# Performance work log

Hardware: AMD Instinct MI355X
Metric: run time of the kernel (lower is better)

The kernel has to match this reference:

```python
import jax, jax.numpy as jnp
import numpy as np

NUM_MODES = 256
IN_FEATURES = 256
OUT_FEATURES = 64
LAYERS = 256   # brick-wall mesh depth
PAIRS = 128    # disjoint adjacent-mode pairs per layer
BATCH = 131072


def setup_inputs() -> dict:
    key = jax.random.key(0)
    kx, kt, kp, ko = jax.random.split(key, 4)
    x = jax.random.normal(kx, (BATCH, IN_FEATURES), dtype=jnp.float32)
    theta = jax.random.uniform(kt, (LAYERS, PAIRS), dtype=jnp.float32, minval=0.0, maxval=float(np.pi))
    phi = jax.random.uniform(kp, (LAYERS, PAIRS), dtype=jnp.float32, minval=0.0, maxval=float(2 * np.pi))
    output_phases = jax.random.uniform(ko, (NUM_MODES,), dtype=jnp.float32, minval=0.0, maxval=float(2 * np.pi))
    # Clements-style brick-wall layout: even layers pair (0,1),(2,3),...;
    # odd layers pair (1,2),(3,4),... with a periodic wrap pair (255,0).
    m1 = np.zeros((LAYERS, PAIRS), np.int32)
    m2 = np.zeros((LAYERS, PAIRS), np.int32)
    for l in range(LAYERS):
        idx = (l % 2 + 2 * np.arange(PAIRS)) % NUM_MODES
        m1[l] = idx
        m2[l] = (idx + 1) % NUM_MODES
    return {
        "x": x,
        "theta": theta,
        "phi": phi,
        "output_phases": output_phases,
        "mode1": jnp.asarray(m1),
        "mode2": jnp.asarray(m2),
    }


def _normalize_optical_params(theta, phi):
    # theta -> [0, pi/2], phi -> [0, 2pi), mirroring normalize_optical_params
    theta = theta % np.pi
    flip = theta > (np.pi / 2)
    theta = jnp.where(flip, np.pi - theta, theta)
    phi = jnp.where(flip, phi + np.pi, phi) % (2.0 * np.pi)
    return theta, phi


def _build_transformation(theta, phi, output_phases, mode1, mode2):
    """Compose the interferometer unitary U = D(out_phases) * T_K * ... * T_1,
    where each T_k is a beamsplitter Givens rotation:
      T[m1,m1]=e^{i phi} cos(t), T[m1,m2]=-sin(t),
      T[m2,m1]=e^{i phi} sin(t), T[m2,m2]= cos(t).
    Pairs within one layer are disjoint, so a whole layer is applied at once."""
    theta, phi = _normalize_optical_params(theta, phi)
    U0 = jnp.eye(NUM_MODES, dtype=jnp.complex64)

    def layer(U, inputs):
        m1, m2, th, ph = inputs              # each [PAIRS]
        r1, r2 = U[m1], U[m2]                # [PAIRS, NUM_MODES]
        e = jnp.exp(1j * ph)[:, None]        # complex64 [PAIRS, 1]
        c = jnp.cos(th)[:, None]
        s = jnp.sin(th)[:, None]
        U = U.at[m1].set(e * c * r1 - s * r2)
        U = U.at[m2].set(e * s * r1 + c * r2)
        return U, None

    U, _ = jax.lax.scan(layer, U0, (mode1, mode2, theta, phi))
    U = jnp.exp(1j * output_phases)[:, None] * U
    return jnp.real(U).astype(jnp.float32)   # [NUM_MODES, NUM_MODES]


def reference(x, theta, phi, output_phases, mode1, mode2):
    T = _build_transformation(theta, phi, output_phases, mode1, mode2)
    # input mask is all-ones (in_features == num_modes); output mask keeps the
    # first OUT_FEATURES modes, then output is sliced to OUT_FEATURES, which
    # is equivalent to using the first OUT_FEATURES rows of T directly.
    T_eff = T[:OUT_FEATURES]                 # [OUT_FEATURES, NUM_MODES]
    return x @ T_eff.T                       # [BATCH, OUT_FEATURES]
```

## Files before the change

kernel.cpp:

```cpp
#include <hip/hip_runtime.h>
#include <hip/hip_bf16.h>
#include <cstdint>
#include <cstddef>

#define PI_F 3.14159265358979323846f
#define TWO_PI_F 6.28318530717958647692f

typedef __bf16 bf16x8 __attribute__((ext_vector_type(8)));
typedef __bf16 bf16x4 __attribute__((ext_vector_type(4)));
typedef float  f32x4  __attribute__((ext_vector_type(4)));

__device__ __forceinline__ __bf16 to_bf16(float f) { return (__bf16)f; }

#define GLD_LDS16(gsrc, ldst)                                            \
  __builtin_amdgcn_global_load_lds(                                      \
      (const __attribute__((address_space(1))) void*)(gsrc),             \
      (__attribute__((address_space(3))) void*)(ldst), 16, 0, 0)

__global__ __launch_bounds__(256) void olk_params(
    const float* __restrict__ theta, const float* __restrict__ phi,
    float4* __restrict__ t4, float2* __restrict__ t2) {
  int idx = blockIdx.x * 256 + threadIdx.x;
  float t = fmodf(theta[idx], PI_F);
  float p = phi[idx];
  if (t > 0.5f * PI_F) { t = PI_F - t; p += PI_F; }
  p = fmodf(p, TWO_PI_F);
  float c  = cosf(t), s  = sinf(t);
  float cp = cosf(p), sp = sinf(p);
  t4[idx] = make_float4(cp * c, sp * c, cp * s, sp * s);
  t2[idx] = make_float2(c, s);
}

struct P8 {
  float4 qa[8];
  float4 qb[8];
  float4 cc[8];
};

template<bool TBL>
__device__ __forceinline__ void loadP8(P8& P, int lb, int lane,
    const float4* __restrict__ t4, const float2* __restrict__ t2,
    const float* __restrict__ theta, const float* __restrict__ phi) {
  if (TBL) {
#pragma unroll
    for (int k = 0; k < 8; ++k) {
      int idx = (lb + k) * 128 + 2 * lane;
      P.qa[k] = t4[idx];
      P.qb[k] = t4[idx + 1];
      P.cc[k] = *(const float4*)&t2[idx];
    }
  } else {
#pragma unroll
    for (int k = 0; k < 8; ++k) {
      int idx = (lb + k) * 128 + 2 * lane;
      float2 th = *(const float2*)&theta[idx];
      float2 ph = *(const float2*)&phi[idx];
      float ta = fmodf(th.x, PI_F), pa = ph.x;
      if (ta > 0.5f * PI_F) { ta = PI_F - ta; pa += PI_F; }
      pa = fmodf(pa, TWO_PI_F);
      float tb = fmodf(th.y, PI_F), pb = ph.y;
      if (tb > 0.5f * PI_F) { tb = PI_F - tb; pb += PI_F; }
      pb = fmodf(pb, TWO_PI_F);
      float ca = cosf(ta), sa = sinf(ta), cpa = cosf(pa), spa = sinf(pa);
      float cb = cosf(tb), sb = sinf(tb), cpb = cosf(pb), spb = sinf(pb);
      P.qa[k] = make_float4(cpa * ca, spa * ca, cpa * sa, spa * sa);
      P.qb[k] = make_float4(cpb * cb, spb * cb, cpb * sb, spb * sb);
      P.cc[k] = make_float4(ca, sa, cb, sb);
    }
  }
}

__device__ __forceinline__ void layer_step(bool odd, int lane,
    float4 qa, float4 qb, float4 cc,
    float& vre0, float& vim0, float& vre1, float& vim1,
    float& vre2, float& vim2, float& vre3, float& vim3) {
  if (!odd) {
    float nr0 = qa.x * vre0 - qa.y * vim0 + qa.z * vre1 - qa.w * vim1;
    float ni0 = qa.x * vim0 + qa.y * vre0 + qa.z * vim1 + qa.w * vre1;
    float nr1 = cc.x * vre1 - cc.y * vre0;
    float ni1 = cc.x * vim1 - cc.y * vim0;
    float nr2 = qb.x * vre2 - qb.y * vim2 + qb.z * vre3 - qb.w * vim3;
    float ni2 = qb.x * vim2 + qb.y * vre2 + qb.z * vim3 + qb.w * vre3;
    float nr3 = cc.z * vre3 - cc.w * vre2;
    float ni3 = cc.z * vim3 - cc.w * vim2;
    vre0 = nr0; vim0 = ni0; vre1 = nr1; vim1 = ni1;
    vre2 = nr2; vim2 = ni2; vre3 = nr3; vim3 = ni3;
  } else {
    int nxt = (lane + 1) & 63, prv = (lane + 63) & 63;
    float xre = __shfl(vre0, nxt, 64);
    float xim = __shfl(vim0, nxt, 64);
    float pre = __shfl(vre3, prv, 64);
    float pim = __shfl(vim3, prv, 64);
    float cp  = __shfl(cc.z, prv, 64);
    float sp  = __shfl(cc.w, prv, 64);
    float nr1 = qa.x * vre1 - qa.y * vim1 + qa.z * vre2 - qa.w * vim2;
    float ni1 = qa.x * vim1 + qa.y * vre1 + qa.z * vim2 + qa.w * vre2;
    float nr2 = cc.x * vre2 - cc.y * vre1;
    float ni2 = cc.x * vim2 - cc.y * vim1;
    float nr3 = qb.x * vre3 - qb.y * vim3 + qb.z * xre - qb.w * xim;
    float ni3 = qb.x * vim3 + qb.y * vre3 + qb.z * xim + qb.w * xre;
    float nr0 = cp * vre0 - sp * pre;
    float ni0 = cp * vim0 - sp * pim;
    vre0 = nr0; vim0 = ni0; vre1 = nr1; vim1 = ni1;
    vre2 = nr2; vim2 = ni2; vre3 = nr3; vim3 = ni3;
  }
}

template<bool TBL>
__global__ __launch_bounds__(256) void olk_build(
    const float* __restrict__ theta, const float* __restrict__ phi,
    const float* __restrict__ outph,
    const float4* __restrict__ t4, const float2* __restrict__ t2,
    __bf16* __restrict__ Tb2) {
  int lane = threadIdx.x & 63;
  int r = blockIdx.x * 4 + (threadIdx.x >> 6);
  int c0 = lane * 4;
  float vre0 = (c0 + 0 == r) ? 1.f : 0.f, vim0 = 0.f;
  float vre1 = (c0 + 1 == r) ? 1.f : 0.f, vim1 = 0.f;
  float vre2 = (c0 + 2 == r) ? 1.f : 0.f, vim2 = 0.f;
  float vre3 = (c0 + 3 == r) ? 1.f : 0.f, vim3 = 0.f;

  P8 A, B;
  loadP8<TBL>(A, 31 * 8, lane, t4, t2, theta, phi);
  for (int it = 0; it < 16; ++it) {
    int bA = 31 - 2 * it;
    int bB = bA - 1;
    loadP8<TBL>(B, bB * 8, lane, t4, t2, theta, phi);
#pragma unroll
    for (int k = 7; k >= 0; --k)
      layer_step((k & 1) != 0, lane, A.qa[k], A.qb[k], A.cc[k],
                 vre0, vim0, vre1, vim1, vre2, vim2, vre3, vim3);
    if (it < 15)
      loadP8<TBL>(A, (bB - 1) * 8, lane, t4, t2, theta, phi);
#pragma unroll
    for (int k = 7; k >= 0; --k)
      layer_step((k & 1) != 0, lane, B.qa[k], B.qb[k], B.cc[k],
                 vre0, vim0, vre1, vim1, vre2, vim2, vre3, vim3);
  }

  float oph = outph[r];
  float co = cosf(oph), so = sinf(oph);
  bf16x4 o;
  o[0] = to_bf16(co * vre0 - so * vim0);
  o[1] = to_bf16(co * vre1 - so * vim1);
  o[2] = to_bf16(co * vre2 - so * vim2);
  o[3] = to_bf16(co * vre3 - so * vim3);

  int ks = lane >> 3, sub = lane & 7;
  int pos = ks * 32 + (sub & 3) * 8 + (sub >> 2) * 4;
  *(bf16x4*)(Tb2 + r * 256 + pos) = o;
}

union FragA { bf16x8 v; };

__global__ __launch_bounds__(256, 4) void olk_mm(
    const float* __restrict__ x, const __bf16* __restrict__ Tb2,
    float* __restrict__ out) {
  __shared__ __bf16 Bl[32 * 512];
  int tid = threadIdx.x, lane = tid & 63, w = tid >> 6;
  int l15 = lane & 15, lg = lane >> 4;

#pragma unroll
  for (int j = 0; j < 8; ++j) {
    int idx = w * 8 + j;
    int ks = idx >> 2, nt = idx & 3;
    const __bf16* src = Tb2 + (nt * 16 + l15) * 256 + ks * 32 + lg * 8;
    GLD_LDS16(src, &Bl[idx * 512]);
  }
  __syncthreads();

#pragma unroll 1
  for (int t = 0; t < 2; ++t) {
    int mt = (blockIdx.x * 4 + w) * 2 + t;
    const float* xr = x + ((size_t)(mt * 16 + l15) << 8) + 4 * lg;

    float4 lo[8], hi[8];
#pragma unroll
    for (int ks = 0; ks < 8; ++ks) {
      lo[ks] = *(const float4*)(xr + ks * 32);
      hi[ks] = *(const float4*)(xr + ks * 32 + 16);
    }

    unsigned bb = 0;
    asm volatile("" : "+v"(bb));

    f32x4 acc[4];
#pragma unroll
    for (int nt = 0; nt < 4; ++nt) acc[nt] = (f32x4){0.f, 0.f, 0.f, 0.f};

#pragma unroll
    for (int ks = 0; ks < 8; ++ks) {
      FragA a;
      a.v[0] = to_bf16(lo[ks].x); a.v[1] = to_bf16(lo[ks].y);
      a.v[2] = to_bf16(lo[ks].z); a.v[3] = to_bf16(lo[ks].w);
      a.v[4] = to_bf16(hi[ks].x); a.v[5] = to_bf16(hi[ks].y);
      a.v[6] = to_bf16(hi[ks].z); a.v[7] = to_bf16(hi[ks].w);
#pragma unroll
      for (int nt = 0; nt < 4; ++nt) {
        bf16x8 bv = *(const bf16x8*)&Bl[bb + (ks * 4 + nt) * 512 + lane * 8];
        acc[nt] = __builtin_amdgcn_mfma_f32_16x16x32_bf16(a.v, bv, acc[nt], 0, 0, 0);
      }
    }

    float* ob = out + ((size_t)mt * 16) * 64 + l15;
#pragma unroll
    for (int r = 0; r < 4; ++r)
#pragma unroll
      for (int nt = 0; nt < 4; ++nt)
        ob[(4 * lg + r) * 64 + nt * 16] = acc[nt][r];
  }
}

extern "C" void kernel_launch(void* const* d_in, const int* in_sizes, int n_in,
                              void* d_out, int out_size, void* d_ws, size_t ws_size,
                              hipStream_t stream) {
  const float* x     = (const float*)d_in[0];
  const float* theta = (const float*)d_in[1];
  const float* phi   = (const float*)d_in[2];
  const float* outph = (const float*)d_in[3];
  float* out = (float*)d_out;

  char* ws = (char*)d_ws;
  bool tbl = ws_size >= (size_t)(832 * 1024);
  float4* t4 = (float4*)ws;
  float2* t2 = (float2*)(ws + 512 * 1024);
  __bf16* Tb2 = (__bf16*)(ws + (tbl ? 768 * 1024 : 0));

  if (tbl) {
    olk_params<<<128, 256, 0, stream>>>(theta, phi, t4, t2);
    olk_build<true><<<16, 256, 0, stream>>>(theta, phi, outph, t4, t2, Tb2);
  } else {
    olk_build<false><<<16, 256, 0, stream>>>(theta, phi, outph, nullptr, nullptr, Tb2);
  }
  olk_mm<<<1024, 256, 0, stream>>>(x, Tb2, out);
}
```

Measured before the change: 83.28 us.

## Restructure GEMM into single-wave persistent blocks with double-buffered LDS x staging

```diff
diff --git a/kernel.cpp b/kernel.cpp
--- a/kernel.cpp
+++ b/kernel.cpp
@@ -151,58 +151,66 @@
   *(bf16x4*)(Tb2 + r * 256 + pos) = o;
 }
 
-union FragA { bf16x8 v; };
-
-__global__ __launch_bounds__(256, 4) void olk_mm(
+#define NTILES 8192
+#define NBLK   1280
+#define TQ     6
+#define TAILB  512
+
+__global__ __launch_bounds__(64) void olk_mm(
     const float* __restrict__ x, const __bf16* __restrict__ Tb2,
     float* __restrict__ out) {
-  __shared__ __bf16 Bl[32 * 512];
-  int tid = threadIdx.x, lane = tid & 63, w = tid >> 6;
-  int l15 = lane & 15, lg = lane >> 4;
-
-#pragma unroll
-  for (int j = 0; j < 8; ++j) {
-    int idx = w * 8 + j;
-    int ks = idx >> 2, nt = idx & 3;
-    const __bf16* src = Tb2 + (nt * 16 + l15) * 256 + ks * 32 + lg * 8;
-    GLD_LDS16(src, &Bl[idx * 512]);
-  }
-  __syncthreads();
-
+  __shared__ float4 sb[2][1024];
+  int lane = threadIdx.x;
+  int l15 = lane & 15, lg = lane >> 4, sw = l15 & 7;
+
+  bf16x8 b[8][4];
+#pragma unroll
+  for (int ks = 0; ks < 8; ++ks)
+#pragma unroll
+    for (int nt = 0; nt < 4; ++nt)
+      b[ks][nt] = *(const bf16x8*)(Tb2 + (nt * 16 + l15) * 256 + ks * 32 + lg * 8);
+  asm volatile("s_waitcnt vmcnt(0)" ::: "memory");
+
+  int bid = blockIdx.x;
+  int start, cnt;
+  if (bid < TAILB) { start = bid * (TQ + 1); cnt = TQ + 1; }
+  else             { start = TAILB * (TQ + 1) + (bid - TAILB) * TQ; cnt = TQ; }
+
+  auto stage = [&](int slot, int tile) {
+    const float* base = x + ((size_t)tile << 12);
+#pragma unroll
+    for (int i = 0; i < 16; ++i) {
+      const float* src = base + i * 256 + ((lane ^ (i & 7)) << 2);
+      GLD_LDS16(src, &sb[slot][i * 64]);
+    }
+  };
+
+  stage(0, start);
 #pragma unroll 1
-  for (int t = 0; t < 2; ++t) {
-    int mt = (blockIdx.x * 4 + w) * 2 + t;
-    const float* xr = x + ((size_t)(mt * 16 + l15) << 8) + 4 * lg;
-
-    float4 lo[8], hi[8];
+  for (int t = 0; t < cnt; ++t) {
+    if (t + 1 < cnt) stage((t + 1) & 1, start + t + 1);
+    asm volatile("s_waitcnt vmcnt(16)" ::: "memory");
+
+    const float4* A = sb[t & 1];
+    f32x4 acc[4];
+#pragma unroll
+    for (int nt = 0; nt < 4; ++nt) acc[nt] = (f32x4){0.f, 0.f, 0.f, 0.f};
+
 #pragma unroll
     for (int ks = 0; ks < 8; ++ks) {
-      lo[ks] = *(const float4*)(xr + ks * 32);
-      hi[ks] = *(const float4*)(xr + ks * 32 + 16);
-    }
-
-    unsigned bb = 0;
-    asm volatile("" : "+v"(bb));
-
-    f32x4 acc[4];
-#pragma unroll
-    for (int nt = 0; nt < 4; ++nt) acc[nt] = (f32x4){0.f, 0.f, 0.f, 0.f};
-
-#pragma unroll
-    for (int ks = 0; ks < 8; ++ks) {
-      FragA a;
-      a.v[0] = to_bf16(lo[ks].x); a.v[1] = to_bf16(lo[ks].y);
-      a.v[2] = to_bf16(lo[ks].z); a.v[3] = to_bf16(lo[ks].w);
-      a.v[4] = to_bf16(hi[ks].x); a.v[5] = to_bf16(hi[ks].y);
-      a.v[6] = to_bf16(hi[ks].z); a.v[7] = to_bf16(hi[ks].w);
-#pragma unroll
-      for (int nt = 0; nt < 4; ++nt) {
-        bf16x8 bv = *(const bf16x8*)&Bl[bb + (ks * 4 + nt) * 512 + lane * 8];
-        acc[nt] = __builtin_amdgcn_mfma_f32_16x16x32_bf16(a.v, bv, acc[nt], 0, 0, 0);
-      }
-    }
-
-    float* ob = out + ((size_t)mt * 16) * 64 + l15;
+      float4 lo = A[l15 * 64 + ((ks * 8 + lg) ^ sw)];
+      float4 hi = A[l15 * 64 + ((ks * 8 + lg + 4) ^ sw)];
+      bf16x8 v;
+      v[0] = to_bf16(lo.x); v[1] = to_bf16(lo.y);
+      v[2] = to_bf16(lo.z); v[3] = to_bf16(lo.w);
+      v[4] = to_bf16(hi.x); v[5] = to_bf16(hi.y);
+      v[6] = to_bf16(hi.z); v[7] = to_bf16(hi.w);
+#pragma unroll
+      for (int nt = 0; nt < 4; ++nt)
+        acc[nt] = __builtin_amdgcn_mfma_f32_16x16x32_bf16(v, b[ks][nt], acc[nt], 0, 0, 0);
+    }
+
+    float* ob = out + ((size_t)(start + t) * 16) * 64 + l15;
 #pragma unroll
     for (int r = 0; r < 4; ++r)
 #pragma unroll
@@ -232,5 +240,5 @@
   } else {
     olk_build<false><<<16, 256, 0, stream>>>(theta, phi, outph, nullptr, nullptr, Tb2);
   }
-  olk_mm<<<1024, 256, 0, stream>>>(x, Tb2, out);
-}
+  olk_mm<<<NBLK, 64, 0, stream>>>(x, Tb2, out);
+}
```

Result: slower. 86.77 us (+4.2%).
